# Optimization experiments

Hardware: AMD Instinct MI355X
Metric: run time of the kernel (lower is better)

Reference implementation:

```python
import jax, jax.numpy as jnp
import numpy as np

B, R, N, D_IN, D_OUT = 8, 4, 1024, 256, 256


def setup_inputs() -> dict:
    key = jax.random.key(0)
    k1, k2, k3, k4 = jax.random.split(key, 4)
    text = jax.random.normal(k1, (B, N, D_IN), dtype=jnp.float32)
    adj = jax.random.uniform(k2, (B, R, N, N), dtype=jnp.float32)
    weight = jax.random.normal(k3, (R, D_IN, D_OUT), dtype=jnp.float32) * 0.02
    bias = jax.random.normal(k4, (D_OUT,), dtype=jnp.float32) * 0.02
    return {"text": text, "adj": adj, "weight": weight, "bias": bias}


def reference(text, adj, weight, bias):
    # Row-normalize adjacency per relation (diag_embed+matmul in torch == row scale).
    rowsum = adj.sum(axis=-1)                                   # [B,R,N]
    r_inv = jnp.where(rowsum == 0, 0.0, 1.0 / rowsum)           # inf -> 0
    norm_adj = adj * r_inv[..., None]                           # [B,R,N,N]
    # Per-relation message passing, batched over relations.
    hidden = jnp.einsum('brij,bjd->brid', norm_adj, text)       # [B,R,N,D_in]
    # Concat over relations along feature dim: [B,N,R*D_in]
    tmp = jnp.transpose(hidden, (0, 2, 1, 3)).reshape(text.shape[0], text.shape[1], -1)
    w = weight.reshape(-1, weight.shape[-1])                    # [R*D_in, D_out]
    return tmp @ w + bias
```

## Files before the change

kernel.cpp:

```cpp
#include <hip/hip_runtime.h>
#include <hip/hip_bf16.h>
#include <stdint.h>

typedef __bf16 bf16_8 __attribute__((ext_vector_type(8)));
typedef float f32x4 __attribute__((ext_vector_type(4)));
typedef unsigned int u32;
typedef unsigned short u16;


__device__ __forceinline__ u16 f2b(float f) {
    return __builtin_bit_cast(u16, __float2bfloat16(f));
}

__device__ __forceinline__ u32 swz_off(u32 row, u32 g) {
    return (row * 4u + (g ^ ((row >> 1) & 3u))) * 16u;
}

__device__ __forceinline__ void gload_lds16(const void* g, void* l) {
    __builtin_amdgcn_global_load_lds((const __attribute__((address_space(1))) void*)g,
                                     (__attribute__((address_space(3))) void*)l, 16, 0, 0);
}

__device__ __forceinline__ void memfence_sched() { asm volatile("" ::: "memory"); }

__device__ __forceinline__ uint4 pack8(float4 a, float4 b) {
    uint4 pk;
    pk.x = (u32)f2b(a.x) | ((u32)f2b(a.y) << 16);
    pk.y = (u32)f2b(a.z) | ((u32)f2b(a.w) << 16);
    pk.z = (u32)f2b(b.x) | ((u32)f2b(b.y) << 16);
    pk.w = (u32)f2b(b.z) | ((u32)f2b(b.w) << 16);
    return pk;
}

template <int KSTEPS>
__device__ __forceinline__ void gemm_core(const u16* pA, u32 strideA,
                                          const u16* pB, u32 strideB,
                                          char* smem, f32x4 acc[4][4]) {
    const u32 t    = threadIdx.x;
    const u32 lane = t & 63u;
    const u32 w    = t >> 6;
    const u32 wm   = (w >> 1) * 64u;
    const u32 wn   = (w & 1u) * 64u;
    const u32 waveByte = (t & 192u) * 16u;
    const u32 row0 = t >> 2;
    const u32 gg0  = (t & 3u) ^ ((row0 >> 1) & 3u);
    const u32 row1 = row0 + 64u;
    const u32 gg1  = ((t + 256u) & 3u) ^ ((row1 >> 1) & 3u);
    const u32 fr = lane & 15u;
    const u32 fg = lane >> 4;

    gload_lds16(pA + (size_t)row0 * strideA + gg0 * 8u, smem + waveByte);
    gload_lds16(pA + (size_t)row1 * strideA + gg1 * 8u, smem + waveByte + 4096u);
    gload_lds16(pB + (size_t)row0 * strideB + gg0 * 8u, smem + 16384u + waveByte);
    gload_lds16(pB + (size_t)row1 * strideB + gg1 * 8u, smem + 16384u + waveByte + 4096u);
    asm volatile("s_waitcnt vmcnt(0)" ::: "memory");
    __builtin_amdgcn_s_barrier();

    u32 c = 0;
#pragma unroll 2
    for (int ks = 0; ks < KSTEPS; ++ks) {
        char* curA = smem + c * 8192u;
        char* curB = smem + 16384u + c * 8192u;
        if (ks + 1 < KSTEPS) {
            char* nxtA = smem + (c ^ 1u) * 8192u;
            char* nxtB = smem + 16384u + (c ^ 1u) * 8192u;
            const u32 k0 = (u32)(ks + 1) * 32u;
            gload_lds16(pA + (size_t)row0 * strideA + k0 + gg0 * 8u, nxtA + waveByte);
            gload_lds16(pA + (size_t)row1 * strideA + k0 + gg1 * 8u, nxtA + waveByte + 4096u);
            gload_lds16(pB + (size_t)row0 * strideB + k0 + gg0 * 8u, nxtB + waveByte);
            gload_lds16(pB + (size_t)row1 * strideB + k0 + gg1 * 8u, nxtB + waveByte + 4096u);
        }

        bf16_8 af[4], bfv[4];
#pragma unroll
        for (int mt = 0; mt < 4; ++mt) {
            uint4 v = *(const uint4*)(curA + swz_off(wm + (u32)mt * 16u + fr, fg));
            af[mt] = __builtin_bit_cast(bf16_8, v);
        }
#pragma unroll
        for (int nt = 0; nt < 4; ++nt) {
            uint4 v = *(const uint4*)(curB + swz_off(wn + (u32)nt * 16u + fr, fg));
            bfv[nt] = __builtin_bit_cast(bf16_8, v);
        }
#pragma unroll
        for (int mt = 0; mt < 4; ++mt)
#pragma unroll
            for (int nt = 0; nt < 4; ++nt)
                acc[mt][nt] = __builtin_amdgcn_mfma_f32_16x16x32_bf16(af[mt], bfv[nt],
                                                                      acc[mt][nt], 0, 0, 0);

        if (ks + 1 < KSTEPS) {
            asm volatile("s_waitcnt vmcnt(0)" ::: "memory");
            __builtin_amdgcn_s_barrier();
        }
        c ^= 1u;
    }
}

__global__ __launch_bounds__(256) void text_cvt_kernel(const float* t, u16* tb) {
    const u32 i8 = blockIdx.x * 256u + threadIdx.x;
    const float4 a = ((const float4*)t)[i8 * 2u];
    const float4 b = ((const float4*)t)[i8 * 2u + 1u];
    ((uint4*)tb)[i8] = pack8(a, b);
}

__global__ __launch_bounds__(256) void wt_cvt_kernel(const float* W, u16* Wt) {
    const u32 idx = blockIdx.x * 256u + threadIdx.x;
    const u32 r = idx >> 16, rem = idx & 65535u, dout = rem >> 8, din = rem & 255u;
    Wt[idx] = f2b(W[(r << 16) + (din << 8) + dout]);
}

__global__ __launch_bounds__(256) void y_gemm_kernel(const u16* Wt, const u16* textb,
                                                     u16* Yt) {
    __shared__ char smem[32768];
    const u32 bx = blockIdx.x;
    const u32 n0 = (bx & 7u) * 128u;
    const u32 m0 = ((bx >> 3) & 1u) * 128u;
    const u32 r  = (bx >> 4) & 3u;
    const u32 b  = bx >> 6;
    const u16* pA = Wt + (size_t)r * 65536u + (size_t)m0 * 256u;
    const u16* pB = textb + (size_t)b * 262144u + (size_t)n0 * 256u;
    f32x4 acc[4][4];
#pragma unroll
    for (int i = 0; i < 4; ++i)
#pragma unroll
        for (int j = 0; j < 4; ++j) acc[i][j] = (f32x4){0.f, 0.f, 0.f, 0.f};
    gemm_core<8>(pA, 256u, pB, 256u, smem, acc);

    const u32 lane = threadIdx.x & 63u, w = threadIdx.x >> 6;
    const u32 wm = (w >> 1) * 64u, wn = (w & 1u) * 64u;
    const u32 rit = (lane >> 4) * 4u, cit = lane & 15u;
    u16* yb = Yt + (size_t)(b * 4u + r) * 262144u;
#pragma unroll
    for (int mt = 0; mt < 4; ++mt)
#pragma unroll
        for (int nt = 0; nt < 4; ++nt) {
            const u32 m = m0 + wm + (u32)mt * 16u + rit;
            const u32 n = n0 + wn + (u32)nt * 16u + cit;
#pragma unroll
            for (int rg = 0; rg < 4; ++rg)
                yb[(size_t)(m + (u32)rg) * 1024u + n] = f2b(acc[mt][nt][rg]);
        }
}

__global__ __launch_bounds__(256) void adj_gemm_fused(const float* adj, const u16* Yt,
                                                      float* partial) {
    __shared__ char smem[33024];
    float* sInv = (float*)(smem + 32768);

    const u32 bxRaw = blockIdx.x;
    const u32 bx = (bxRaw & 7u) * 128u + (bxRaw >> 3);

    const u32 n0 = (bx & 1u) * 128u;
    const u32 m0 = ((bx >> 1) & 15u) * 64u;
    const u32 r  = (bx >> 5) & 3u;
    const u32 b  = bx >> 7;

    const float* pA = adj + (size_t)(b * 4u + r) * 1048576u + (size_t)m0 * 1024u;
    const u16*   pB = Yt + (size_t)(b * 4u + r) * 262144u + (size_t)n0 * 1024u;

    const u32 t    = threadIdx.x;
    const u32 lane = t & 63u;
    const u32 w    = t >> 6;
    const u32 wm   = (w >> 1) * 32u;
    const u32 wn   = (w & 1u) * 64u;
    const u32 waveByte = (t & 192u) * 16u;
    const u32 rowA = t >> 2;
    const u32 ggA  = (t & 3u) ^ ((rowA >> 1) & 3u);
    const u32 rowB1 = rowA + 64u;
    const u32 ggB1  = ((t + 256u) & 3u) ^ ((rowB1 >> 1) & 3u);
    const u32 fr = lane & 15u;
    const u32 fg = lane >> 4;

    f32x4 acc[2][4];
#pragma unroll
    for (int i = 0; i < 2; ++i)
#pragma unroll
        for (int j = 0; j < 4; ++j) acc[i][j] = (f32x4){0.f, 0.f, 0.f, 0.f};

    const float* rp0 = pA + (size_t)rowA * 1024u + ggA * 8u;

    float s0 = 0.f;
    float4 rA[2][2];

    auto do_mfma = [&](char* curA, char* curB) {
        bf16_8 af[2], bfv[4];
#pragma unroll
        for (int mt = 0; mt < 2; ++mt) {
            uint4 v = *(const uint4*)(curA + swz_off(wm + (u32)mt * 16u + fr, fg));
            af[mt] = __builtin_bit_cast(bf16_8, v);
        }
#pragma unroll
        for (int nt = 0; nt < 4; ++nt) {
            uint4 v = *(const uint4*)(curB + swz_off(wn + (u32)nt * 16u + fr, fg));
            bfv[nt] = __builtin_bit_cast(bf16_8, v);
        }
#pragma unroll
        for (int mt = 0; mt < 2; ++mt)
#pragma unroll
            for (int nt = 0; nt < 4; ++nt)
                acc[mt][nt] = __builtin_amdgcn_mfma_f32_16x16x32_bf16(af[mt], bfv[nt],
                                                                      acc[mt][nt], 0, 0, 0);
    };
    auto pack_to = [&](const float4* rs, char* dst) {
        const float4 a0 = rs[0], a1 = rs[1];
        s0 += (a0.x + a0.y + a0.z + a0.w) + (a1.x + a1.y + a1.z + a1.w);
        *(uint4*)(dst + t * 16u) = pack8(a0, a1);
    };

    rA[0][0] = *(const float4*)(rp0);
    rA[0][1] = *(const float4*)(rp0 + 4);
    gload_lds16(pB + (size_t)rowA * 1024u + ggA * 8u, smem + 8192u + waveByte);
    gload_lds16(pB + (size_t)rowB1 * 1024u + ggB1 * 8u, smem + 8192u + waveByte + 4096u);
    memfence_sched();
    rA[1][0] = *(const float4*)(rp0 + 32u);
    rA[1][1] = *(const float4*)(rp0 + 36u);
    gload_lds16(pB + (size_t)rowA * 1024u + 32u + ggA * 8u, smem + 16384u + waveByte);
    gload_lds16(pB + (size_t)rowB1 * 1024u + 32u + ggB1 * 8u, smem + 16384u + waveByte + 4096u);
    memfence_sched();
    pack_to(rA[0], smem);
    asm volatile("s_waitcnt vmcnt(4) lgkmcnt(0)" ::: "memory");
    __builtin_amdgcn_s_barrier();

#pragma unroll 6
    for (int ks = 0; ks < 30; ++ks) {
        const int cA = ks & 1;
        const int nA = cA ^ 1;
        char* bufAc = smem + (u32)cA * 4096u;
        char* bufAn = smem + (u32)nA * 4096u;
        char* bufBc = smem + 8192u + (u32)(ks % 3) * 8192u;
        char* bufBn = smem + 8192u + (u32)((ks + 2) % 3) * 8192u;

        pack_to(rA[nA], bufAn);

        const u32 k2 = (u32)(ks + 2) * 32u;
        rA[cA][0] = *(const float4*)(rp0 + k2);
        rA[cA][1] = *(const float4*)(rp0 + k2 + 4u);
        gload_lds16(pB + (size_t)rowA * 1024u + k2 + ggA * 8u, bufBn + waveByte);
        gload_lds16(pB + (size_t)rowB1 * 1024u + k2 + ggB1 * 8u, bufBn + waveByte + 4096u);

        do_mfma(bufAc, bufBc);

        asm volatile("s_waitcnt vmcnt(4) lgkmcnt(0)" ::: "memory");
        __builtin_amdgcn_s_barrier();
    }

    pack_to(rA[1], smem + 4096u);
    do_mfma(smem + 0u, smem + 8192u);
    asm volatile("s_waitcnt vmcnt(0) lgkmcnt(0)" ::: "memory");
    __builtin_amdgcn_s_barrier();

    do_mfma(smem + 4096u, smem + 16384u);

    s0 += __shfl_down(s0, 2, 64); s0 += __shfl_down(s0, 1, 64);
    if ((t & 3u) == 0u) {
        sInv[rowA] = (s0 == 0.f) ? 0.f : 1.f / s0;
    }
    __syncthreads();

    const u32 rit = (lane >> 4) * 4u, cit = lane & 15u;
    float* pp = partial + (size_t)(b * 4u + r) * 262144u;
#pragma unroll
    for (int mt = 0; mt < 2; ++mt) {
        const u32 mBase = wm + (u32)mt * 16u + rit;
        float sv[4];
#pragma unroll
        for (int rg = 0; rg < 4; ++rg) sv[rg] = sInv[mBase + (u32)rg];
#pragma unroll
        for (int nt = 0; nt < 4; ++nt) {
            const u32 n = n0 + wn + (u32)nt * 16u + cit;
#pragma unroll
            for (int rg = 0; rg < 4; ++rg)
                pp[(size_t)(m0 + mBase + (u32)rg) * 256u + n] = acc[mt][nt][rg] * sv[rg];
        }
    }
}

__global__ __launch_bounds__(256) void reduce_kernel(const float* partial,
                                                     const float* bias, float* out) {
    const u32 i4 = blockIdx.x * 256u + threadIdx.x;
    const u32 base = i4 * 4u;
    const u32 b = base >> 18;
    const u32 rem = base & 262143u;
    float4 s = ((const float4*)bias)[i4 & 63u];
#pragma unroll
    for (u32 r = 0; r < 4; ++r) {
        const float4 v = *(const float4*)(partial + (((size_t)(b * 4u + r)) << 18) + rem);
        s.x += v.x; s.y += v.y; s.z += v.z; s.w += v.w;
    }
    ((float4*)out)[i4] = s;
}

extern "C" void kernel_launch(void* const* d_in, const int* in_sizes, int n_in,
                              void* d_out, int out_size, void* d_ws, size_t ws_size,
                              hipStream_t stream) {
    const float* text = (const float*)d_in[0];
    const float* adj  = (const float*)d_in[1];
    const float* wgt  = (const float*)d_in[2];
    const float* bias = (const float*)d_in[3];
    float* out = (float*)d_out;

    char* ws = (char*)d_ws;
    u16* Yt        = (u16*)ws;
    u16* textb     = (u16*)(ws + 16777216u);
    u16* Wt        = (u16*)(ws + 20971520u);
    float* partial = (float*)(ws + 21495808u);

    text_cvt_kernel<<<1024, 256, 0, stream>>>(text, textb);
    wt_cvt_kernel<<<1024, 256, 0, stream>>>(wgt, Wt);
    y_gemm_kernel<<<512, 256, 0, stream>>>(Wt, textb, Yt);
    adj_gemm_fused<<<1024, 256, 0, stream>>>(adj, Yt, partial);
    reduce_kernel<<<2048, 256, 0, stream>>>(partial, bias, out);
}
```

Before: 68.42 us.

## Give each adj-GEMM block the full output width so adj is read once

```diff
diff --git a/kernel.cpp b/kernel.cpp
--- a/kernel.cpp
+++ b/kernel.cpp
@@ -143,136 +143,120 @@
         }
 }
 
-__global__ __launch_bounds__(256) void adj_gemm_fused(const float* adj, const u16* Yt,
-                                                      float* partial) {
-    __shared__ char smem[33024];
-    float* sInv = (float*)(smem + 32768);
-
-    const u32 bxRaw = blockIdx.x;
-    const u32 bx = (bxRaw & 7u) * 128u + (bxRaw >> 3);
-
-    const u32 n0 = (bx & 1u) * 128u;
-    const u32 m0 = ((bx >> 1) & 15u) * 64u;
-    const u32 r  = (bx >> 5) & 3u;
-    const u32 b  = bx >> 7;
-
-    const float* pA = adj + (size_t)(b * 4u + r) * 1048576u + (size_t)m0 * 1024u;
-    const u16*   pB = Yt + (size_t)(b * 4u + r) * 262144u + (size_t)n0 * 1024u;
+__global__ __launch_bounds__(512, 4) void adj_gemm_partial(const float* adj,
+                                                           const u16* Yt,
+                                                           float* partial) {
+    __shared__ char smem[57600];
+    char* bufA = smem;
+    char* bufB = smem + 8192;
+    float* sInv = (float*)(smem + 57344);
+
+    const u32 raw = blockIdx.x;
+    const u32 bx = (raw & 7u) * 64u + (raw >> 3);
+
+    const u32 i0 = (bx & 15u) * 64u;
+    const u32 r  = (bx >> 4) & 3u;
+    const u32 b  = bx >> 6;
+
+    const float* pA = adj + (size_t)(b * 4u + r) * 1048576u + (size_t)i0 * 1024u;
+    const u16*   pB = Yt + (size_t)(b * 4u + r) * 262144u;
 
     const u32 t    = threadIdx.x;
     const u32 lane = t & 63u;
     const u32 w    = t >> 6;
-    const u32 wm   = (w >> 1) * 32u;
-    const u32 wn   = (w & 1u) * 64u;
-    const u32 waveByte = (t & 192u) * 16u;
-    const u32 rowA = t >> 2;
-    const u32 ggA  = (t & 3u) ^ ((rowA >> 1) & 3u);
-    const u32 rowB1 = rowA + 64u;
-    const u32 ggB1  = ((t + 256u) & 3u) ^ ((rowB1 >> 1) & 3u);
-    const u32 fr = lane & 15u;
-    const u32 fg = lane >> 4;
-
-    f32x4 acc[2][4];
-#pragma unroll
-    for (int i = 0; i < 2; ++i)
-#pragma unroll
-        for (int j = 0; j < 4; ++j) acc[i][j] = (f32x4){0.f, 0.f, 0.f, 0.f};
-
-    const float* rp0 = pA + (size_t)rowA * 1024u + ggA * 8u;
+    const u32 wi   = (w >> 1) * 16u;
+    const u32 wd   = (w & 1u) * 128u;
+    const u32 fr   = lane & 15u;
+    const u32 fg   = lane >> 4;
+
+    const u32 arow = t >> 3;
+    const u32 acg  = ((t >> 1) & 3u) ^ ((arow >> 1) & 3u);
+    const float* aPtr = pA + (size_t)arow * 1024u + acg * 8u + (t & 1u) * 4u;
+
+    const u32 brow0 = t >> 2;
+    const u32 brow1 = (t + 512u) >> 2;
+    const u32 bcg0  = (t & 3u) ^ ((brow0 >> 1) & 3u);
+    const u32 bcg1  = (t & 3u) ^ ((brow1 >> 1) & 3u);
+    const u16* bPtr0 = pB + (size_t)brow0 * 1024u + bcg0 * 8u;
+    const u16* bPtr1 = pB + (size_t)brow1 * 1024u + bcg1 * 8u;
+    const u32 waveB = (t & 448u) * 16u;
+
+    f32x4 acc[8];
+#pragma unroll
+    for (int i = 0; i < 8; ++i) acc[i] = (f32x4){0.f, 0.f, 0.f, 0.f};
 
     float s0 = 0.f;
-    float4 rA[2][2];
-
+    float4 rA[2];
+
+    auto stageB = [&](u32 kt, char* dst) {
+        gload_lds16(bPtr0 + kt * 32u, dst + waveB);
+        gload_lds16(bPtr1 + kt * 32u, dst + 8192u + waveB);
+    };
+    auto packA = [&](float4 a, char* dst) {
+        s0 += (a.x + a.y) + (a.z + a.w);
+        uint2 pk;
+        pk.x = (u32)f2b(a.x) | ((u32)f2b(a.y) << 16);
+        pk.y = (u32)f2b(a.z) | ((u32)f2b(a.w) << 16);
+        *(uint2*)(dst + t * 8u) = pk;
+    };
     auto do_mfma = [&](char* curA, char* curB) {
-        bf16_8 af[2], bfv[4];
-#pragma unroll
-        for (int mt = 0; mt < 2; ++mt) {
-            uint4 v = *(const uint4*)(curA + swz_off(wm + (u32)mt * 16u + fr, fg));
-            af[mt] = __builtin_bit_cast(bf16_8, v);
-        }
-#pragma unroll
-        for (int nt = 0; nt < 4; ++nt) {
-            uint4 v = *(const uint4*)(curB + swz_off(wn + (u32)nt * 16u + fr, fg));
-            bfv[nt] = __builtin_bit_cast(bf16_8, v);
-        }
-#pragma unroll
-        for (int mt = 0; mt < 2; ++mt)
-#pragma unroll
-            for (int nt = 0; nt < 4; ++nt)
-                acc[mt][nt] = __builtin_amdgcn_mfma_f32_16x16x32_bf16(af[mt], bfv[nt],
-                                                                      acc[mt][nt], 0, 0, 0);
+        uint4 va = *(const uint4*)(curA + swz_off(wi + fr, fg));
+        bf16_8 af = __builtin_bit_cast(bf16_8, va);
+#pragma unroll
+        for (int nt = 0; nt < 8; ++nt) {
+            uint4 v = *(const uint4*)(curB + swz_off(wd + (u32)nt * 16u + fr, fg));
+            bf16_8 bfv = __builtin_bit_cast(bf16_8, v);
+            acc[nt] = __builtin_amdgcn_mfma_f32_16x16x32_bf16(af, bfv, acc[nt], 0, 0, 0);
+        }
     };
-    auto pack_to = [&](const float4* rs, char* dst) {
-        const float4 a0 = rs[0], a1 = rs[1];
-        s0 += (a0.x + a0.y + a0.z + a0.w) + (a1.x + a1.y + a1.z + a1.w);
-        *(uint4*)(dst + t * 16u) = pack8(a0, a1);
-    };
-
-    rA[0][0] = *(const float4*)(rp0);
-    rA[0][1] = *(const float4*)(rp0 + 4);
-    gload_lds16(pB + (size_t)rowA * 1024u + ggA * 8u, smem + 8192u + waveByte);
-    gload_lds16(pB + (size_t)rowB1 * 1024u + ggB1 * 8u, smem + 8192u + waveByte + 4096u);
+
+    rA[0] = *(const float4*)(aPtr);
+    stageB(0u, bufB);
     memfence_sched();
-    rA[1][0] = *(const float4*)(rp0 + 32u);
-    rA[1][1] = *(const float4*)(rp0 + 36u);
-    gload_lds16(pB + (size_t)rowA * 1024u + 32u + ggA * 8u, smem + 16384u + waveByte);
-    gload_lds16(pB + (size_t)rowB1 * 1024u + 32u + ggB1 * 8u, smem + 16384u + waveByte + 4096u);
+    rA[1] = *(const float4*)(aPtr + 32u);
+    stageB(1u, bufB + 16384u);
     memfence_sched();
-    pack_to(rA[0], smem);
-    asm volatile("s_waitcnt vmcnt(4) lgkmcnt(0)" ::: "memory");
+    packA(rA[0], bufA);
+    asm volatile("s_waitcnt vmcnt(3) lgkmcnt(0)" ::: "memory");
     __builtin_amdgcn_s_barrier();
 
 #pragma unroll 6
     for (int ks = 0; ks < 30; ++ks) {
         const int cA = ks & 1;
         const int nA = cA ^ 1;
-        char* bufAc = smem + (u32)cA * 4096u;
-        char* bufAn = smem + (u32)nA * 4096u;
-        char* bufBc = smem + 8192u + (u32)(ks % 3) * 8192u;
-        char* bufBn = smem + 8192u + (u32)((ks + 2) % 3) * 8192u;
-
-        pack_to(rA[nA], bufAn);
-
-        const u32 k2 = (u32)(ks + 2) * 32u;
-        rA[cA][0] = *(const float4*)(rp0 + k2);
-        rA[cA][1] = *(const float4*)(rp0 + k2 + 4u);
-        gload_lds16(pB + (size_t)rowA * 1024u + k2 + ggA * 8u, bufBn + waveByte);
-        gload_lds16(pB + (size_t)rowB1 * 1024u + k2 + ggB1 * 8u, bufBn + waveByte + 4096u);
-
-        do_mfma(bufAc, bufBc);
-
-        asm volatile("s_waitcnt vmcnt(4) lgkmcnt(0)" ::: "memory");
+
+        packA(rA[nA], bufA + (u32)nA * 4096u);
+        rA[cA] = *(const float4*)(aPtr + (u32)(ks + 2) * 32u);
+        stageB((u32)(ks + 2), bufB + (u32)((ks + 2) % 3) * 16384u);
+
+        do_mfma(bufA + (u32)cA * 4096u, bufB + (u32)(ks % 3) * 16384u);
+
+        asm volatile("s_waitcnt vmcnt(3) lgkmcnt(0)" ::: "memory");
         __builtin_amdgcn_s_barrier();
     }
 
-    pack_to(rA[1], smem + 4096u);
-    do_mfma(smem + 0u, smem + 8192u);
+    packA(rA[1], bufA + 4096u);
+    do_mfma(bufA, bufB);
     asm volatile("s_waitcnt vmcnt(0) lgkmcnt(0)" ::: "memory");
     __builtin_amdgcn_s_barrier();
 
-    do_mfma(smem + 4096u, smem + 16384u);
-
-    s0 += __shfl_down(s0, 2, 64); s0 += __shfl_down(s0, 1, 64);
-    if ((t & 3u) == 0u) {
-        sInv[rowA] = (s0 == 0.f) ? 0.f : 1.f / s0;
-    }
+    do_mfma(bufA + 4096u, bufB + 16384u);
+
+    s0 += __shfl_down(s0, 4, 64);
+    s0 += __shfl_down(s0, 2, 64);
+    s0 += __shfl_down(s0, 1, 64);
+    if ((t & 7u) == 0u) sInv[arow] = (s0 == 0.f) ? 0.f : 1.f / s0;
     __syncthreads();
 
-    const u32 rit = (lane >> 4) * 4u, cit = lane & 15u;
-    float* pp = partial + (size_t)(b * 4u + r) * 262144u;
-#pragma unroll
-    for (int mt = 0; mt < 2; ++mt) {
-        const u32 mBase = wm + (u32)mt * 16u + rit;
-        float sv[4];
-#pragma unroll
-        for (int rg = 0; rg < 4; ++rg) sv[rg] = sInv[mBase + (u32)rg];
-#pragma unroll
-        for (int nt = 0; nt < 4; ++nt) {
-            const u32 n = n0 + wn + (u32)nt * 16u + cit;
-#pragma unroll
-            for (int rg = 0; rg < 4; ++rg)
-                pp[(size_t)(m0 + mBase + (u32)rg) * 256u + n] = acc[mt][nt][rg] * sv[rg];
-        }
+    const u32 rit = fg * 4u;
+    float* pp = partial + (size_t)(b * 4u + r) * 262144u + (size_t)i0 * 256u;
+#pragma unroll
+    for (int rg = 0; rg < 4; ++rg) {
+        const u32 mRow = wi + rit + (u32)rg;
+        const float inv = sInv[mRow];
+#pragma unroll
+        for (int nt = 0; nt < 8; ++nt)
+            pp[(size_t)mRow * 256u + wd + (u32)nt * 16u + fr] = acc[nt][rg] * inv;
     }
 }
 
@@ -309,6 +293,6 @@
     text_cvt_kernel<<<1024, 256, 0, stream>>>(text, textb);
     wt_cvt_kernel<<<1024, 256, 0, stream>>>(wgt, Wt);
     y_gemm_kernel<<<512, 256, 0, stream>>>(Wt, textb, Yt);
-    adj_gemm_fused<<<1024, 256, 0, stream>>>(adj, Yt, partial);
+    adj_gemm_partial<<<512, 512, 0, stream>>>(adj, Yt, partial);
     reduce_kernel<<<2048, 256, 0, stream>>>(partial, bias, out);
 }
```

Result: no change. 67.09 us (-1.9%).
